# Kernel optimization log

Hardware: AMD Instinct MI355X
Metric: run time of the kernel (lower is better)

## Reference

```python
import jax, jax.numpy as jnp
import numpy as np

VOCAB = 50257
D_EMB = 1024
N_NODES = 4096

def setup_inputs() -> dict:
    key = jax.random.key(0)
    k1, k2, k3 = jax.random.split(key, 3)
    x = jax.random.normal(k1, (N_NODES, D_EMB), dtype=jnp.float32)
    W = jax.random.normal(k2, (VOCAB, D_EMB), dtype=jnp.float32) * 0.02
    y = jax.random.randint(k3, (N_NODES,), 0, VOCAB, dtype=jnp.int64)
    return {"x": x, "W": W, "y": y}

def reference(x, W, y):
    # Decoder: logits = x @ W.T  -> (n_nodes, vocab)
    logits = jnp.einsum('nd,vd->nv', x, W)
    # CrossEntropyLoss (mean reduction)
    logp = jax.nn.log_softmax(logits, axis=-1)
    nll = -jnp.take_along_axis(logp, y[:, None], axis=-1)[:, 0]
    return jnp.mean(nll)
```

## Files before the change

kernel.cpp:

```cpp
#include <hip/hip_runtime.h>
#include <hip/hip_bf16.h>
#include <math.h>


#define N_NODES 4096
#define D_EMB   1024
#define VOCAB   50257
#define VPAD    50432
#define NT      197
#define KT      16

typedef __attribute__((ext_vector_type(8))) short short8;
typedef __attribute__((ext_vector_type(4))) float f32x4;

__device__ __forceinline__ unsigned short f2bf(float f) {
  unsigned int x = __float_as_uint(f);
  x += 0x7fffu + ((x >> 16) & 1u);
  return (unsigned short)(x >> 16);
}

__global__ void cvt_w_kernel(const float* __restrict__ W, unsigned short* __restrict__ Wb) {
  const long long total = (long long)VPAD * (D_EMB / 8);
  for (long long gid = (long long)blockIdx.x * 256 + threadIdx.x; gid < total;
       gid += (long long)gridDim.x * 256) {
    long long e = gid << 3;
    int row = (int)(e >> 10);
    short8 o;
    if (row < VOCAB) {
      const float4* p = (const float4*)(W + e);
      float4 u = p[0];
      float4 v = p[1];
      o[0] = (short)f2bf(u.x); o[1] = (short)f2bf(u.y); o[2] = (short)f2bf(u.z); o[3] = (short)f2bf(u.w);
      o[4] = (short)f2bf(v.x); o[5] = (short)f2bf(v.y); o[6] = (short)f2bf(v.z); o[7] = (short)f2bf(v.w);
    } else {
      o[0]=0; o[1]=0; o[2]=0; o[3]=0; o[4]=0; o[5]=0; o[6]=0; o[7]=0;
    }
    *(short8*)(Wb + e) = o;
  }
}

__global__ void cvt_x_kernel(const float* __restrict__ x, unsigned short* __restrict__ Xb) {
  long long gid = (long long)blockIdx.x * 256 + threadIdx.x;
  long long e = gid << 3;
  const float4* p = (const float4*)(x + e);
  float4 u = p[0];
  float4 v = p[1];
  short8 o;
  o[0] = (short)f2bf(u.x); o[1] = (short)f2bf(u.y); o[2] = (short)f2bf(u.z); o[3] = (short)f2bf(u.w);
  o[4] = (short)f2bf(v.x); o[5] = (short)f2bf(v.y); o[6] = (short)f2bf(v.z); o[7] = (short)f2bf(v.w);
  *(short8*)(Xb + e) = o;
}

#define MFMAQ(Q)                                                                      \
  do {                                                                                \
    _Pragma("unroll")                                                                 \
    for (int ni = 0; ni < 4; ++ni) {                                                  \
      _Pragma("unroll")                                                               \
      for (int kk = 0; kk < 2; ++kk) {                                                \
        acc[2*(Q)  ][ni] = __builtin_amdgcn_mfma_f32_16x16x32_bf16(af[0][kk], bf[ni][kk], acc[2*(Q)  ][ni], 0, 0, 0); \
        acc[2*(Q)+1][ni] = __builtin_amdgcn_mfma_f32_16x16x32_bf16(af[1][kk], bf[ni][kk], acc[2*(Q)+1][ni], 0, 0, 0); \
      }                                                                               \
    }                                                                                 \
  } while (0)

#define STAGE_A(U, P)                                                                 \
  do {                                                                               \
    const int _b = (U) & 1;                                                          \
    const long long _ko = (long long)(U) * 64;                                       \
    _Pragma("unroll")                                                                \
    for (int h = 0; h < 2; ++h)                                                      \
      __builtin_amdgcn_global_load_lds(                                              \
          (const __attribute__((address_space(1))) void*)(Xb + abase[h][P] + _ko),   \
          (__attribute__((address_space(3))) void*)(sh + _b*32768 + h*8192 + (P)*4096 + dst0), \
          16, 0, 0);                                                                 \
  } while (0)
#define STAGE_B(U, P)                                                                 \
  do {                                                                               \
    const int _b = (U) & 1;                                                          \
    const long long _ko = (long long)(U) * 64;                                       \
    _Pragma("unroll")                                                                \
    for (int h = 0; h < 2; ++h)                                                      \
      __builtin_amdgcn_global_load_lds(                                              \
          (const __attribute__((address_space(1))) void*)(Wb + bbase[h][P] + _ko),   \
          (__attribute__((address_space(3))) void*)(sh + _b*32768 + 16384 + h*8192 + (P)*4096 + dst0), \
          16, 0, 0);                                                                 \
  } while (0)

#define PHASE_OPEN()                                   \
  __builtin_amdgcn_s_barrier();                        \
  asm volatile("s_waitcnt lgkmcnt(0)" ::: "memory");   \
  __builtin_amdgcn_sched_barrier(0);                   \
  __builtin_amdgcn_s_setprio(1)
#define PHASE_CLOSE()                                  \
  __builtin_amdgcn_s_setprio(0);                       \
  __builtin_amdgcn_s_barrier()

__global__ __launch_bounds__(512, 2) void gemm_stats_kernel(
    const unsigned short* __restrict__ Xb,
    const unsigned short* __restrict__ Wb,
    float2* __restrict__ partials)
{
  __shared__ __align__(16) unsigned short sh[65536];

  const int tid  = threadIdx.x;
  const int lane = tid & 63;
  const int wid  = tid >> 6;
  const int wr   = wid >> 2;
  const int wcol = wid & 3;
  const int g    = lane >> 4;
  const int r16  = lane & 15;

  const int bm0 = blockIdx.x * 256;
  const int bn0 = blockIdx.y * 256;

  const int srb = tid >> 3;
  const int scg = ((tid & 7) << 3) ^ ((srb & 7) << 3);
  const int dst0 = tid * 8;
  long long abase[2][2], bbase[2][2];
  #pragma unroll
  for (int h = 0; h < 2; ++h)
    #pragma unroll
    for (int p = 0; p < 2; ++p) {
      abase[h][p] = (long long)(bm0 + h*128 + p*64 + srb) * D_EMB + scg;
      bbase[h][p] = (long long)(bn0 + h*128 + p*64 + srb) * D_EMB + scg;
    }

  f32x4 acc[8][4];
  #pragma unroll
  for (int m = 0; m < 8; ++m)
    #pragma unroll
    for (int n = 0; n < 4; ++n)
      #pragma unroll
      for (int j = 0; j < 4; ++j)
        acc[m][n][j] = 0.f;

  const int arow = wr * 128 + r16;
  const int brow = wcol * 64 + r16;
  const int sw   = (r16 & 7) << 3;
  const int colp0 = (g * 8) ^ sw;
  const int colp1 = (32 + g * 8) ^ sw;

  STAGE_A(0, 0); STAGE_A(0, 1); STAGE_B(0, 0); STAGE_B(0, 1);
  STAGE_A(1, 0);
  asm volatile("s_waitcnt vmcnt(2)" ::: "memory");
  __builtin_amdgcn_s_barrier();

  for (int u = 0; u < KT; ++u) {
    const unsigned short* Ab = sh + (u & 1) * 32768;
    const unsigned short* Bb = Ab + 16384;
    short8 bf[4][2], af[2][2];

    #pragma unroll
    for (int ni = 0; ni < 4; ++ni) {
      bf[ni][0] = *(const short8*)(Bb + (brow + ni*16)*64 + colp0);
      bf[ni][1] = *(const short8*)(Bb + (brow + ni*16)*64 + colp1);
    }
    #pragma unroll
    for (int i = 0; i < 2; ++i) {
      af[i][0] = *(const short8*)(Ab + (arow + i*16)*64 + colp0);
      af[i][1] = *(const short8*)(Ab + (arow + i*16)*64 + colp1);
    }
    if (u + 1 < KT) STAGE_A(u + 1, 1);
    PHASE_OPEN();
    MFMAQ(0);
    PHASE_CLOSE();

    #pragma unroll
    for (int i = 0; i < 2; ++i) {
      af[i][0] = *(const short8*)(Ab + (arow + (2+i)*16)*64 + colp0);
      af[i][1] = *(const short8*)(Ab + (arow + (2+i)*16)*64 + colp1);
    }
    if (u + 1 < KT) STAGE_B(u + 1, 0);
    PHASE_OPEN();
    MFMAQ(1);
    PHASE_CLOSE();

    #pragma unroll
    for (int i = 0; i < 2; ++i) {
      af[i][0] = *(const short8*)(Ab + (arow + (4+i)*16)*64 + colp0);
      af[i][1] = *(const short8*)(Ab + (arow + (4+i)*16)*64 + colp1);
    }
    if (u + 1 < KT) STAGE_B(u + 1, 1);
    if (u + 2 < KT) STAGE_A(u + 2, 0);
    PHASE_OPEN();
    MFMAQ(2);
    PHASE_CLOSE();

    #pragma unroll
    for (int i = 0; i < 2; ++i) {
      af[i][0] = *(const short8*)(Ab + (arow + (6+i)*16)*64 + colp0);
      af[i][1] = *(const short8*)(Ab + (arow + (6+i)*16)*64 + colp1);
    }
    __builtin_amdgcn_s_barrier();
    asm volatile("s_waitcnt lgkmcnt(0)" ::: "memory");
    __builtin_amdgcn_sched_barrier(0);
    __builtin_amdgcn_s_setprio(1);
    MFMAQ(3);
    __builtin_amdgcn_s_setprio(0);
    if (u < KT - 2) {
      asm volatile("s_waitcnt vmcnt(2)" ::: "memory");
      __builtin_amdgcn_s_barrier();
    } else if (u == KT - 2) {
      asm volatile("s_waitcnt vmcnt(0)" ::: "memory");
      __builtin_amdgcn_s_barrier();
    }
  }

  float2 (*stats)[4] = (float2 (*)[4])sh;
  #pragma unroll
  for (int mi = 0; mi < 8; ++mi) {
    #pragma unroll
    for (int j = 0; j < 4; ++j) {
      float vmax = -INFINITY;
      #pragma unroll
      for (int ni = 0; ni < 4; ++ni) {
        const int colg = bn0 + wcol*64 + ni*16 + r16;
        float v = (colg < VOCAB) ? acc[mi][ni][j] : -INFINITY;
        vmax = fmaxf(vmax, v);
      }
      vmax = fmaxf(vmax, __shfl_xor(vmax, 1));
      vmax = fmaxf(vmax, __shfl_xor(vmax, 2));
      vmax = fmaxf(vmax, __shfl_xor(vmax, 4));
      vmax = fmaxf(vmax, __shfl_xor(vmax, 8));
      float ssum = 0.f;
      #pragma unroll
      for (int ni = 0; ni < 4; ++ni) {
        const int colg = bn0 + wcol*64 + ni*16 + r16;
        if (colg < VOCAB) ssum += __expf(acc[mi][ni][j] - vmax);
      }
      ssum += __shfl_xor(ssum, 1);
      ssum += __shfl_xor(ssum, 2);
      ssum += __shfl_xor(ssum, 4);
      ssum += __shfl_xor(ssum, 8);
      if (r16 == 0) {
        stats[wr*128 + mi*16 + g*4 + j][wcol] = make_float2(vmax, ssum);
      }
    }
  }
  __syncthreads();
  if (tid < 256) {
    float2 a0 = stats[tid][0], a1 = stats[tid][1], a2 = stats[tid][2], a3 = stats[tid][3];
    float M = fmaxf(fmaxf(a0.x, a1.x), fmaxf(a2.x, a3.x));
    float S = a0.y * __expf(a0.x - M) + a1.y * __expf(a1.x - M)
            + a2.y * __expf(a2.x - M) + a3.y * __expf(a3.x - M);
    partials[(long long)(bm0 + tid) * NT + blockIdx.y] = make_float2(M, S);
  }
}

__global__ void lse_kernel(const float2* __restrict__ partials,
                           const float* __restrict__ x,
                           const float* __restrict__ W,
                           const int* __restrict__ y,
                           float* __restrict__ row_nll) {
  const int n = blockIdx.x * 4 + (threadIdx.x >> 6);
  const int l = threadIdx.x & 63;
  const float2* pr = partials + (long long)n * NT;
  float M = -INFINITY, S = 0.f;
  for (int t = l; t < NT; t += 64) {
    float2 p = pr[t];
    float nM = fmaxf(M, p.x);
    S = S * __expf(M - nM) + p.y * __expf(p.x - nM);
    M = nM;
  }
  const float4* xr = (const float4*)(x + ((long long)n << 10));
  const float4* wv = (const float4*)(W + ((long long)y[n] << 10));
  float dot = 0.f;
  #pragma unroll
  for (int i = 0; i < 4; ++i) {
    float4 a = xr[l + 64*i];
    float4 b = wv[l + 64*i];
    dot = fmaf(a.x, b.x, fmaf(a.y, b.y, fmaf(a.z, b.z, fmaf(a.w, b.w, dot))));
  }
  #pragma unroll
  for (int off = 1; off < 64; off <<= 1) {
    float Mo = __shfl_xor(M, off);
    float So = __shfl_xor(S, off);
    float nM = fmaxf(M, Mo);
    S = S * __expf(M - nM) + So * __expf(Mo - nM);
    M = nM;
    dot += __shfl_xor(dot, off);
  }
  if (l == 0) row_nll[n] = (M + logf(S)) - dot;
}

__global__ void mean_kernel(const float* __restrict__ row_nll, float* __restrict__ out) {
  __shared__ float red[4];
  float s = 0.f;
  for (int i = threadIdx.x; i < N_NODES; i += 256) s += row_nll[i];
  #pragma unroll
  for (int m = 32; m; m >>= 1) s += __shfl_xor(s, m, 64);
  if ((threadIdx.x & 63) == 0) red[threadIdx.x >> 6] = s;
  __syncthreads();
  if (threadIdx.x == 0) out[0] = (red[0] + red[1] + red[2] + red[3]) * (1.0f / N_NODES);
}

extern "C" void kernel_launch(void* const* d_in, const int* in_sizes, int n_in,
                              void* d_out, int out_size, void* d_ws, size_t ws_size,
                              hipStream_t stream) {
  const float* x = (const float*)d_in[0];
  const float* W = (const float*)d_in[1];
  const int*   y = (const int*)d_in[2];
  float* out = (float*)d_out;

  char* ws = (char*)d_ws;
  unsigned short* Wb = (unsigned short*)ws;
  unsigned short* Xb = (unsigned short*)(ws + 103284736);
  float2* partials   = (float2*)(ws + 111673344);
  float* logit_y     = (float*)(ws + 118128640);
  float* row_nll     = (float*)(ws + 118145024);
  (void)logit_y;

  hipLaunchKernelGGL(cvt_w_kernel, dim3(2048), dim3(256), 0, stream, W, Wb);
  hipLaunchKernelGGL(cvt_x_kernel, dim3(N_NODES * (D_EMB / 8) / 256), dim3(256), 0, stream, x, Xb);
  hipLaunchKernelGGL(gemm_stats_kernel, dim3(16, NT), dim3(512), 0, stream, Xb, Wb, partials);
  hipLaunchKernelGGL(lse_kernel, dim3(N_NODES / 4), dim3(256), 0, stream, partials, x, W, y, row_nll);
  hipLaunchKernelGGL(mean_kernel, dim3(1), dim3(256), 0, stream, row_nll, out);
}
```

Measured before the change: 796.7 us.

## Restructure GEMM main loop to triple-buffered K=32 tiles with register double-buffering

Result: slower. 1.418 ms (+77.9%).

```diff
diff --git a/kernel.cpp b/kernel.cpp
--- a/kernel.cpp
+++ b/kernel.cpp
@@ -8,7 +8,7 @@
 #define VOCAB   50257
 #define VPAD    50432
 #define NT      197
-#define KT      16
+#define KT32    32
 
 typedef __attribute__((ext_vector_type(8))) short short8;
 typedef __attribute__((ext_vector_type(4))) float f32x4;
@@ -19,88 +19,92 @@
   return (unsigned short)(x >> 16);
 }
 
-__global__ void cvt_w_kernel(const float* __restrict__ W, unsigned short* __restrict__ Wb) {
-  const long long total = (long long)VPAD * (D_EMB / 8);
-  for (long long gid = (long long)blockIdx.x * 256 + threadIdx.x; gid < total;
+__global__ void cvt_kernel(const float* __restrict__ x, const float* __restrict__ W,
+                           unsigned short* __restrict__ Xb, unsigned short* __restrict__ Wb) {
+  const long long XG  = (long long)N_NODES * (D_EMB / 8);
+  const long long TOT = XG + (long long)VPAD * (D_EMB / 8);
+  for (long long gid = (long long)blockIdx.x * 256 + threadIdx.x; gid < TOT;
        gid += (long long)gridDim.x * 256) {
-    long long e = gid << 3;
-    int row = (int)(e >> 10);
     short8 o;
-    if (row < VOCAB) {
-      const float4* p = (const float4*)(W + e);
-      float4 u = p[0];
-      float4 v = p[1];
-      o[0] = (short)f2bf(u.x); o[1] = (short)f2bf(u.y); o[2] = (short)f2bf(u.z); o[3] = (short)f2bf(u.w);
-      o[4] = (short)f2bf(v.x); o[5] = (short)f2bf(v.y); o[6] = (short)f2bf(v.z); o[7] = (short)f2bf(v.w);
+    if (gid < XG) {
+      long long e = gid << 3;
+      const float4* p = (const float4*)(x + e);
+      float4 u = p[0], v = p[1];
+      o[0]=(short)f2bf(u.x); o[1]=(short)f2bf(u.y); o[2]=(short)f2bf(u.z); o[3]=(short)f2bf(u.w);
+      o[4]=(short)f2bf(v.x); o[5]=(short)f2bf(v.y); o[6]=(short)f2bf(v.z); o[7]=(short)f2bf(v.w);
+      *(short8*)(Xb + e) = o;
     } else {
-      o[0]=0; o[1]=0; o[2]=0; o[3]=0; o[4]=0; o[5]=0; o[6]=0; o[7]=0;
+      long long wg = gid - XG;
+      long long e = wg << 3;
+      int row = (int)(e >> 10);
+      if (row < VOCAB) {
+        const float4* p = (const float4*)(W + e);
+        float4 u = p[0], v = p[1];
+        o[0]=(short)f2bf(u.x); o[1]=(short)f2bf(u.y); o[2]=(short)f2bf(u.z); o[3]=(short)f2bf(u.w);
+        o[4]=(short)f2bf(v.x); o[5]=(short)f2bf(v.y); o[6]=(short)f2bf(v.z); o[7]=(short)f2bf(v.w);
+      } else {
+        o[0]=0;o[1]=0;o[2]=0;o[3]=0;o[4]=0;o[5]=0;o[6]=0;o[7]=0;
+      }
+      *(short8*)(Wb + e) = o;
     }
-    *(short8*)(Wb + e) = o;
-  }
-}
-
-__global__ void cvt_x_kernel(const float* __restrict__ x, unsigned short* __restrict__ Xb) {
-  long long gid = (long long)blockIdx.x * 256 + threadIdx.x;
-  long long e = gid << 3;
-  const float4* p = (const float4*)(x + e);
-  float4 u = p[0];
-  float4 v = p[1];
-  short8 o;
-  o[0] = (short)f2bf(u.x); o[1] = (short)f2bf(u.y); o[2] = (short)f2bf(u.z); o[3] = (short)f2bf(u.w);
-  o[4] = (short)f2bf(v.x); o[5] = (short)f2bf(v.y); o[6] = (short)f2bf(v.z); o[7] = (short)f2bf(v.w);
-  *(short8*)(Xb + e) = o;
-}
-
-#define MFMAQ(Q)                                                                      \
-  do {                                                                                \
-    _Pragma("unroll")                                                                 \
-    for (int ni = 0; ni < 4; ++ni) {                                                  \
-      _Pragma("unroll")                                                               \
-      for (int kk = 0; kk < 2; ++kk) {                                                \
-        acc[2*(Q)  ][ni] = __builtin_amdgcn_mfma_f32_16x16x32_bf16(af[0][kk], bf[ni][kk], acc[2*(Q)  ][ni], 0, 0, 0); \
-        acc[2*(Q)+1][ni] = __builtin_amdgcn_mfma_f32_16x16x32_bf16(af[1][kk], bf[ni][kk], acc[2*(Q)+1][ni], 0, 0, 0); \
-      }                                                                               \
-    }                                                                                 \
-  } while (0)
-
-#define STAGE_A(U, P)                                                                 \
-  do {                                                                               \
-    const int _b = (U) & 1;                                                          \
-    const long long _ko = (long long)(U) * 64;                                       \
-    _Pragma("unroll")                                                                \
-    for (int h = 0; h < 2; ++h)                                                      \
-      __builtin_amdgcn_global_load_lds(                                              \
-          (const __attribute__((address_space(1))) void*)(Xb + abase[h][P] + _ko),   \
-          (__attribute__((address_space(3))) void*)(sh + _b*32768 + h*8192 + (P)*4096 + dst0), \
-          16, 0, 0);                                                                 \
-  } while (0)
-#define STAGE_B(U, P)                                                                 \
-  do {                                                                               \
-    const int _b = (U) & 1;                                                          \
-    const long long _ko = (long long)(U) * 64;                                       \
-    _Pragma("unroll")                                                                \
-    for (int h = 0; h < 2; ++h)                                                      \
-      __builtin_amdgcn_global_load_lds(                                              \
-          (const __attribute__((address_space(1))) void*)(Wb + bbase[h][P] + _ko),   \
-          (__attribute__((address_space(3))) void*)(sh + _b*32768 + 16384 + h*8192 + (P)*4096 + dst0), \
-          16, 0, 0);                                                                 \
-  } while (0)
-
-#define PHASE_OPEN()                                   \
-  __builtin_amdgcn_s_barrier();                        \
-  asm volatile("s_waitcnt lgkmcnt(0)" ::: "memory");   \
-  __builtin_amdgcn_sched_barrier(0);                   \
-  __builtin_amdgcn_s_setprio(1)
-#define PHASE_CLOSE()                                  \
-  __builtin_amdgcn_s_setprio(0);                       \
-  __builtin_amdgcn_s_barrier()
+  }
+}
+
+#define GLD(SRC, DST)                                                              \
+  __builtin_amdgcn_global_load_lds(                                                \
+      (const __attribute__((address_space(1))) void*)(SRC),                        \
+      (__attribute__((address_space(3))) void*)(DST), 16, 0, 0)
+
+#define STAGE_T(U, BB)                                                             \
+  do {                                                                             \
+    const int _ko = (U) << 5;                                                      \
+    GLD(Xb + aoff0 + _ko,          sh + (BB) + dstA);                              \
+    GLD(Xb + aoff0 + 131072 + _ko, sh + (BB) + 4096 + dstA);                       \
+    GLD(Wb + boff0 + _ko,          sh + (BB) + 8192 + dstA);                       \
+    GLD(Wb + boff0 + 131072 + _ko, sh + (BB) + 12288 + dstA);                      \
+  } while (0)
+
+#define READ_FRAGS(BB, FA, FB)                                                     \
+  do {                                                                             \
+    const unsigned short* _A = sh + (BB) + aread;                                  \
+    const unsigned short* _B = sh + (BB) + bread;                                  \
+    _Pragma("unroll")                                                              \
+    for (int ni = 0; ni < 4; ++ni) FB[ni] = *(const short8*)(_B + ni * 512);       \
+    _Pragma("unroll")                                                              \
+    for (int mi = 0; mi < 8; ++mi) FA[mi] = *(const short8*)(_A + mi * 512);       \
+  } while (0)
+
+#define MFMA32(FA, FB)                                                             \
+  do {                                                                             \
+    _Pragma("unroll")                                                              \
+    for (int mi = 0; mi < 8; ++mi)                                                 \
+      _Pragma("unroll")                                                            \
+      for (int ni = 0; ni < 4; ++ni)                                               \
+        acc[mi][ni] = __builtin_amdgcn_mfma_f32_16x16x32_bf16(FA[mi], FB[ni], acc[mi][ni], 0, 0, 0); \
+  } while (0)
+
+#define TILE(U, FCA, FCB, FNA, FNB)                                                \
+  do {                                                                             \
+    if ((U) + 2 < KT32) STAGE_T((U) + 2, bstage);                                  \
+    if ((U) + 1 < KT32) {                                                          \
+      if ((U) < KT32 - 2) { asm volatile("s_waitcnt vmcnt(4)" ::: "memory"); }     \
+      else                { asm volatile("s_waitcnt vmcnt(0)" ::: "memory"); }     \
+      __builtin_amdgcn_s_barrier();                                                \
+      READ_FRAGS(bnext, FNA, FNB);                                                 \
+      __builtin_amdgcn_sched_barrier(0);                                           \
+    }                                                                              \
+    __builtin_amdgcn_s_setprio(1);                                                 \
+    MFMA32(FCA, FCB);                                                              \
+    __builtin_amdgcn_s_setprio(0);                                                 \
+    { int _t = bcur; bcur = bnext; bnext = bstage; bstage = _t; }                  \
+  } while (0)
 
 __global__ __launch_bounds__(512, 2) void gemm_stats_kernel(
     const unsigned short* __restrict__ Xb,
     const unsigned short* __restrict__ Wb,
     float2* __restrict__ partials)
 {
-  __shared__ __align__(16) unsigned short sh[65536];
+  __shared__ __align__(16) unsigned short sh[49152];
 
   const int tid  = threadIdx.x;
   const int lane = tid & 63;
@@ -113,17 +117,16 @@
   const int bm0 = blockIdx.x * 256;
   const int bn0 = blockIdx.y * 256;
 
-  const int srb = tid >> 3;
-  const int scg = ((tid & 7) << 3) ^ ((srb & 7) << 3);
-  const int dst0 = tid * 8;
-  long long abase[2][2], bbase[2][2];
-  #pragma unroll
-  for (int h = 0; h < 2; ++h)
-    #pragma unroll
-    for (int p = 0; p < 2; ++p) {
-      abase[h][p] = (long long)(bm0 + h*128 + p*64 + srb) * D_EMB + scg;
-      bbase[h][p] = (long long)(bn0 + h*128 + p*64 + srb) * D_EMB + scg;
-    }
+  const int cgu   = (tid & 7) ^ ((tid >> 3) & 7);
+  const int rl0   = ((tid >> 3) << 1) | (cgu >> 2);
+  const int cgc   = (cgu & 3) << 3;
+  const int aoff0 = (bm0 + rl0) * D_EMB + cgc;
+  const int boff0 = (bn0 + rl0) * D_EMB + cgc;
+  const int dstA  = tid * 8;
+
+  const int cgr   = (((r16 & 1) << 2) | g) ^ (r16 >> 1);
+  const int aread = (wr * 64 + (r16 >> 1)) * 64 + cgr * 8;
+  const int bread = 8192 + (wcol * 32 + (r16 >> 1)) * 64 + cgr * 8;
 
   f32x4 acc[8][4];
   #pragma unroll
@@ -134,76 +137,19 @@
       for (int j = 0; j < 4; ++j)
         acc[m][n][j] = 0.f;
 
-  const int arow = wr * 128 + r16;
-  const int brow = wcol * 64 + r16;
-  const int sw   = (r16 & 7) << 3;
-  const int colp0 = (g * 8) ^ sw;
-  const int colp1 = (32 + g * 8) ^ sw;
-
-  STAGE_A(0, 0); STAGE_A(0, 1); STAGE_B(0, 0); STAGE_B(0, 1);
-  STAGE_A(1, 0);
-  asm volatile("s_waitcnt vmcnt(2)" ::: "memory");
+  short8 af_a[8], bf_a[4], af_b[8], bf_b[4];
+  int bcur = 0, bnext = 16384, bstage = 32768;
+
+  STAGE_T(0, 0);
+  STAGE_T(1, 16384);
+  asm volatile("s_waitcnt vmcnt(4)" ::: "memory");
   __builtin_amdgcn_s_barrier();
-
-  for (int u = 0; u < KT; ++u) {
-    const unsigned short* Ab = sh + (u & 1) * 32768;
-    const unsigned short* Bb = Ab + 16384;
-    short8 bf[4][2], af[2][2];
-
-    #pragma unroll
-    for (int ni = 0; ni < 4; ++ni) {
-      bf[ni][0] = *(const short8*)(Bb + (brow + ni*16)*64 + colp0);
-      bf[ni][1] = *(const short8*)(Bb + (brow + ni*16)*64 + colp1);
-    }
-    #pragma unroll
-    for (int i = 0; i < 2; ++i) {
-      af[i][0] = *(const short8*)(Ab + (arow + i*16)*64 + colp0);
-      af[i][1] = *(const short8*)(Ab + (arow + i*16)*64 + colp1);
-    }
-    if (u + 1 < KT) STAGE_A(u + 1, 1);
-    PHASE_OPEN();
-    MFMAQ(0);
-    PHASE_CLOSE();
-
-    #pragma unroll
-    for (int i = 0; i < 2; ++i) {
-      af[i][0] = *(const short8*)(Ab + (arow + (2+i)*16)*64 + colp0);
-      af[i][1] = *(const short8*)(Ab + (arow + (2+i)*16)*64 + colp1);
-    }
-    if (u + 1 < KT) STAGE_B(u + 1, 0);
-    PHASE_OPEN();
-    MFMAQ(1);
-    PHASE_CLOSE();
-
-    #pragma unroll
-    for (int i = 0; i < 2; ++i) {
-      af[i][0] = *(const short8*)(Ab + (arow + (4+i)*16)*64 + colp0);
-      af[i][1] = *(const short8*)(Ab + (arow + (4+i)*16)*64 + colp1);
-    }
-    if (u + 1 < KT) STAGE_B(u + 1, 1);
-    if (u + 2 < KT) STAGE_A(u + 2, 0);
-    PHASE_OPEN();
-    MFMAQ(2);
-    PHASE_CLOSE();
-
-    #pragma unroll
-    for (int i = 0; i < 2; ++i) {
-      af[i][0] = *(const short8*)(Ab + (arow + (6+i)*16)*64 + colp0);
-      af[i][1] = *(const short8*)(Ab + (arow + (6+i)*16)*64 + colp1);
-    }
-    __builtin_amdgcn_s_barrier();
-    asm volatile("s_waitcnt lgkmcnt(0)" ::: "memory");
-    __builtin_amdgcn_sched_barrier(0);
-    __builtin_amdgcn_s_setprio(1);
-    MFMAQ(3);
-    __builtin_amdgcn_s_setprio(0);
-    if (u < KT - 2) {
-      asm volatile("s_waitcnt vmcnt(2)" ::: "memory");
-      __builtin_amdgcn_s_barrier();
-    } else if (u == KT - 2) {
-      asm volatile("s_waitcnt vmcnt(0)" ::: "memory");
-      __builtin_amdgcn_s_barrier();
-    }
+  READ_FRAGS(0, af_a, bf_a);
+
+  #pragma unroll 2
+  for (int v = 0; v < KT32; v += 2) {
+    TILE(v,     af_a, bf_a, af_b, bf_b);
+    TILE(v + 1, af_b, bf_b, af_a, bf_a);
   }
 
   float2 (*stats)[4] = (float2 (*)[4])sh;
@@ -214,7 +160,7 @@
       float vmax = -INFINITY;
       #pragma unroll
       for (int ni = 0; ni < 4; ++ni) {
-        const int colg = bn0 + wcol*64 + ni*16 + r16;
+        const int colg = bn0 + wcol * 64 + ni * 16 + r16;
         float v = (colg < VOCAB) ? acc[mi][ni][j] : -INFINITY;
         vmax = fmaxf(vmax, v);
       }
@@ -225,7 +171,7 @@
       float ssum = 0.f;
       #pragma unroll
       for (int ni = 0; ni < 4; ++ni) {
-        const int colg = bn0 + wcol*64 + ni*16 + r16;
+        const int colg = bn0 + wcol * 64 + ni * 16 + r16;
         if (colg < VOCAB) ssum += __expf(acc[mi][ni][j] - vmax);
       }
       ssum += __shfl_xor(ssum, 1);
@@ -233,7 +179,7 @@
       ssum += __shfl_xor(ssum, 4);
       ssum += __shfl_xor(ssum, 8);
       if (r16 == 0) {
-        stats[wr*128 + mi*16 + g*4 + j][wcol] = make_float2(vmax, ssum);
+        stats[wr * 128 + mi * 16 + g * 4 + j][wcol] = make_float2(vmax, ssum);
       }
     }
   }
@@ -267,8 +213,8 @@
   float dot = 0.f;
   #pragma unroll
   for (int i = 0; i < 4; ++i) {
-    float4 a = xr[l + 64*i];
-    float4 b = wv[l + 64*i];
+    float4 a = xr[l + 64 * i];
+    float4 b = wv[l + 64 * i];
     dot = fmaf(a.x, b.x, fmaf(a.y, b.y, fmaf(a.z, b.z, fmaf(a.w, b.w, dot))));
   }
   #pragma unroll
@@ -306,12 +252,9 @@
   unsigned short* Wb = (unsigned short*)ws;
   unsigned short* Xb = (unsigned short*)(ws + 103284736);
   float2* partials   = (float2*)(ws + 111673344);
-  float* logit_y     = (float*)(ws + 118128640);
   float* row_nll     = (float*)(ws + 118145024);
-  (void)logit_y;
-
-  hipLaunchKernelGGL(cvt_w_kernel, dim3(2048), dim3(256), 0, stream, W, Wb);
-  hipLaunchKernelGGL(cvt_x_kernel, dim3(N_NODES * (D_EMB / 8) / 256), dim3(256), 0, stream, x, Xb);
+
+  hipLaunchKernelGGL(cvt_kernel, dim3(2048), dim3(256), 0, stream, x, W, Xb, Wb);
   hipLaunchKernelGGL(gemm_stats_kernel, dim3(16, NT), dim3(512), 0, stream, Xb, Wb, partials);
   hipLaunchKernelGGL(lse_kernel, dim3(N_NODES / 4), dim3(256), 0, stream, partials, x, W, y, row_nll);
   hipLaunchKernelGGL(mean_kernel, dim3(1), dim3(256), 0, stream, row_nll, out);
```
